# Optimization experiments

Hardware: AMD Instinct MI355X
Metric: run time of the kernel (lower is better)

Reference implementation:

```python
import jax, jax.numpy as jnp
import numpy as np

RHO, MU, DT = 1.0, 0.1, 4.0
AX_X, AX_Y = -1, -2  # x = last axis, y = second-to-last


def first_derivative(f, ax, scheme):
    # unit grid spacing; boundary wrap is irrelevant since [1:-1,1:-1] is sliced off
    if scheme == 'left':
        return f - jnp.roll(f, 1, ax)
    if scheme == 'right':
        return jnp.roll(f, -1, ax) - f
    return 0.5 * (jnp.roll(f, -1, ax) - jnp.roll(f, 1, ax))  # central


def vel_map(f, ax, side):
    # staggered-grid interpolation of velocity to neighboring face
    if side == 'left':
        return 0.5 * (f + jnp.roll(f, 1, ax))
    return 0.5 * (f + jnp.roll(f, -1, ax))


def laplacian(f):
    return (jnp.roll(f, 1, AX_X) + jnp.roll(f, -1, AX_X)
            + jnp.roll(f, 1, AX_Y) + jnp.roll(f, -1, AX_Y) - 4.0 * f)


def setup_inputs() -> dict:
    key = jax.random.key(0)
    k1, k2, k3, k4 = jax.random.split(key, 4)
    B, H, W = 8, 1024, 1024
    return {
        'v_old': jax.random.normal(k1, (B, 2, H, W), dtype=jnp.float32),
        'v_new': jax.random.normal(k2, (B, 2, H, W), dtype=jnp.float32),
        'p_new': jax.random.normal(k3, (B, 1, H, W), dtype=jnp.float32),
        'flow_mask_mac': jax.random.randint(k4, (B, 1, H, W), 0, 2).astype(jnp.int32),
    }


def reference(v_old, v_new, p_new, flow_mask_mac):
    mask = flow_mask_mac.astype(v_old.dtype)
    v = 0.5 * (v_new + v_old)  # integration == 'imex'

    u_old, w_old = v_old[:, 0:1], v_old[:, 1:2]
    u_new, w_new = v_new[:, 0:1], v_new[:, 1:2]
    u, w = v[:, 0:1], v[:, 1:2]

    # x-momentum residual (channel 1)
    res_x = mask * (RHO * ((w_new - w_old) / DT
                           + w * first_derivative(w, AX_X, 'central')
                           + 0.5 * (vel_map(u, AX_X, 'left') * first_derivative(w, AX_Y, 'left')
                                    + vel_map(u, AX_X, 'right') * first_derivative(w, AX_Y, 'right')))
                    + first_derivative(p_new, AX_X, 'left')
                    - MU * laplacian(w))

    # y-momentum residual (channel 0)
    res_y = mask * (RHO * ((u_new - u_old) / DT
                           + u * first_derivative(u, AX_Y, 'central')
                           + 0.5 * (vel_map(w, AX_Y, 'left') * first_derivative(u, AX_X, 'left')
                                    + vel_map(w, AX_Y, 'right') * first_derivative(u, AX_X, 'right')))
                    + first_derivative(p_new, AX_Y, 'left')
                    - MU * laplacian(u))

    loss_x = jnp.mean(jnp.square(res_x)[:, :, 1:-1, 1:-1], axis=(1, 2, 3))
    loss_y = jnp.mean(jnp.square(res_y)[:, :, 1:-1, 1:-1], axis=(1, 2, 3))
    return loss_x + loss_y  # shape [B]
```

## Files before the change

### kernel.cpp

```cpp
#include <hip/hip_runtime.h>


#define NS_H 1024
#define NS_W 1024
#define RPB 2
#define PAIRS ((NS_H - 2) / RPB)
#define PARTS_PER_B PAIRS

__device__ __forceinline__ float4 ld4(const float* p) { return *(const float4*)p; }
__device__ __forceinline__ int4  ld4i(const int* p)   { return *(const int4*)p; }
__device__ __forceinline__ float4 avg4(float4 a, float4 b) {
    return make_float4(0.5f*(a.x+b.x), 0.5f*(a.y+b.y), 0.5f*(a.z+b.z), 0.5f*(a.w+b.w));
}
__device__ __forceinline__ float4 sub4(float4 a, float4 b) {
    return make_float4(a.x-b.x, a.y-b.y, a.z-b.z, a.w-b.w);
}

__global__ __launch_bounds__(256, 3) void ns_loss_partial(
    const float* __restrict__ v_old,
    const float* __restrict__ v_new,
    const float* __restrict__ p,
    const int*   __restrict__ mask,
    float* __restrict__ ws)
{
    const int blkp = blockIdx.x;
    const int lg   = (blkp & 7) * PAIRS + (blkp >> 3);
    const int b    = lg / PAIRS;
    const int pr   = lg % PAIRS;
    const int y    = 1 + pr * RPB;

    const size_t hw = (size_t)NS_H * NS_W;
    const float* uo = v_old + (size_t)b * 2 * hw;
    const float* wo = uo + hw;
    const float* un = v_new + (size_t)b * 2 * hw;
    const float* wn = un + hw;
    const float* pb = p    + (size_t)b * hw;
    const int*   mb = mask + (size_t)b * hw;

    const int tid  = (int)threadIdx.x;
    const int lane = tid & 63;
    const int wid  = tid >> 6;
    const int x0   = tid * 4;
    const bool has_r = (x0 + 4 < NS_W);

    const int rm  = (y - 1) * NS_W;
    const int rc  = y * NS_W;
    const int rp  = rc + NS_W;
    const int rpp = rp + NS_W;

    float4 un_m = ld4(un + rm  + x0), uo_m = ld4(uo + rm  + x0);
    float4 un_c = ld4(un + rc  + x0), uo_c = ld4(uo + rc  + x0);
    float4 un_p = ld4(un + rp  + x0), uo_p = ld4(uo + rp  + x0);
    float4 un_q = ld4(un + rpp + x0), uo_q = ld4(uo + rpp + x0);
    float4 wn_m = ld4(wn + rm  + x0), wo_m = ld4(wo + rm  + x0);
    float4 wn_c = ld4(wn + rc  + x0), wo_c = ld4(wo + rc  + x0);
    float4 wn_p = ld4(wn + rp  + x0), wo_p = ld4(wo + rp  + x0);
    float4 wn_q = ld4(wn + rpp + x0), wo_q = ld4(wo + rpp + x0);
    float4 p_m4 = ld4(pb + rm + x0);
    float4 p_c4 = ld4(pb + rc + x0);
    float4 p_p4 = ld4(pb + rp + x0);
    int4   m_c4 = ld4i(mb + rc + x0);
    int4   m_p4 = ld4i(mb + rp + x0);
    __builtin_amdgcn_sched_barrier(0);

    float4 u_m = avg4(un_m, uo_m), u_c = avg4(un_c, uo_c);
    float4 u_p = avg4(un_p, uo_p), u_q = avg4(un_q, uo_q);
    float4 w_m = avg4(wn_m, wo_m), w_c = avg4(wn_c, wo_c);
    float4 w_p = avg4(wn_p, wo_p), w_q = avg4(wn_q, wo_q);
    float4 du_c = sub4(un_c, uo_c), du_p = sub4(un_p, uo_p);
    float4 dw_c = sub4(wn_c, wo_c), dw_p = sub4(wn_p, wo_p);

    __shared__ float edge[4][10];
    if (lane == 63) {
        edge[wid][0] = u_c.w;  edge[wid][1] = w_c.w;  edge[wid][2] = p_c4.w;
        edge[wid][3] = u_p.w;  edge[wid][4] = w_p.w;  edge[wid][5] = p_p4.w;
    }
    if (lane == 0) {
        edge[wid][6] = u_c.x;  edge[wid][7] = w_c.x;
        edge[wid][8] = u_p.x;  edge[wid][9] = w_p.x;
    }
    __syncthreads();

    float ul_c = __shfl_up(u_c.w, 1),  wl_c = __shfl_up(w_c.w, 1);
    float ul_p = __shfl_up(u_p.w, 1),  wl_p = __shfl_up(w_p.w, 1);
    float pl_c = __shfl_up(p_c4.w, 1), pl_p = __shfl_up(p_p4.w, 1);
    if (lane == 0 && wid > 0) {
        ul_c = edge[wid-1][0]; wl_c = edge[wid-1][1]; pl_c = edge[wid-1][2];
        ul_p = edge[wid-1][3]; wl_p = edge[wid-1][4]; pl_p = edge[wid-1][5];
    }
    float ur_c = __shfl_down(u_c.x, 1), wr_c = __shfl_down(w_c.x, 1);
    float ur_p = __shfl_down(u_p.x, 1), wr_p = __shfl_down(w_p.x, 1);
    if (lane == 63 && wid < 3) {
        ur_c = edge[wid+1][6]; wr_c = edge[wid+1][7];
        ur_p = edge[wid+1][8]; wr_p = edge[wid+1][9];
    }
    if (!has_r) { ur_c = 0.f; wr_c = 0.f; ur_p = 0.f; wr_p = 0.f; }

    float acc = 0.f;

    {
        const float uc[6]  = {ul_c, u_c.x, u_c.y, u_c.z, u_c.w, ur_c};
        const float wcv[6] = {wl_c, w_c.x, w_c.y, w_c.z, w_c.w, wr_c};
        const float uym[4] = {u_m.x, u_m.y, u_m.z, u_m.w};
        const float uyp[4] = {u_p.x, u_p.y, u_p.z, u_p.w};
        const float wym[4] = {w_m.x, w_m.y, w_m.z, w_m.w};
        const float wyp[4] = {w_p.x, w_p.y, w_p.z, w_p.w};
        const float du[4]  = {du_c.x, du_c.y, du_c.z, du_c.w};
        const float dw[4]  = {dw_c.x, dw_c.y, dw_c.z, dw_c.w};
        const float pcv[5] = {pl_c, p_c4.x, p_c4.y, p_c4.z, p_c4.w};
        const float pym[4] = {p_m4.x, p_m4.y, p_m4.z, p_m4.w};
        const int   mm[4]  = {m_c4.x, m_c4.y, m_c4.z, m_c4.w};

        #pragma unroll
        for (int j = 0; j < 4; ++j) {
            const int x = x0 + j;
            const float m = (x >= 1 && x <= NS_W - 2) ? (float)mm[j] : 0.f;
            const float u_cc = uc[j+1],  u_xm = uc[j],  u_xp = uc[j+2];
            const float w_cc = wcv[j+1], w_xm = wcv[j], w_xp = wcv[j+2];

            float res_x =
                dw[j] * 0.25f
              + w_cc * 0.5f * (w_xp - w_xm)
              + 0.5f * ( 0.5f * (u_cc + u_xm) * (w_cc   - wym[j])
                       + 0.5f * (u_cc + u_xp) * (wyp[j] - w_cc  ) )
              + (pcv[j+1] - pcv[j])
              - 0.1f * (w_xm + w_xp + wym[j] + wyp[j] - 4.f * w_cc);

            float res_y =
                du[j] * 0.25f
              + u_cc * 0.5f * (uyp[j] - uym[j])
              + 0.5f * ( 0.5f * (w_cc + wym[j]) * (u_cc - u_xm)
                       + 0.5f * (w_cc + wyp[j]) * (u_xp - u_cc) )
              + (pcv[j+1] - pym[j])
              - 0.1f * (u_xm + u_xp + uym[j] + uyp[j] - 4.f * u_cc);

            acc += m * (res_x * res_x + res_y * res_y);
        }
    }

    {
        const float uc[6]  = {ul_p, u_p.x, u_p.y, u_p.z, u_p.w, ur_p};
        const float wcv[6] = {wl_p, w_p.x, w_p.y, w_p.z, w_p.w, wr_p};
        const float uym[4] = {u_c.x, u_c.y, u_c.z, u_c.w};
        const float uyp[4] = {u_q.x, u_q.y, u_q.z, u_q.w};
        const float wym[4] = {w_c.x, w_c.y, w_c.z, w_c.w};
        const float wyp[4] = {w_q.x, w_q.y, w_q.z, w_q.w};
        const float du[4]  = {du_p.x, du_p.y, du_p.z, du_p.w};
        const float dw[4]  = {dw_p.x, dw_p.y, dw_p.z, dw_p.w};
        const float pcv[5] = {pl_p, p_p4.x, p_p4.y, p_p4.z, p_p4.w};
        const float pym[4] = {p_c4.x, p_c4.y, p_c4.z, p_c4.w};
        const int   mm[4]  = {m_p4.x, m_p4.y, m_p4.z, m_p4.w};

        #pragma unroll
        for (int j = 0; j < 4; ++j) {
            const int x = x0 + j;
            const float m = (x >= 1 && x <= NS_W - 2) ? (float)mm[j] : 0.f;
            const float u_cc = uc[j+1],  u_xm = uc[j],  u_xp = uc[j+2];
            const float w_cc = wcv[j+1], w_xm = wcv[j], w_xp = wcv[j+2];

            float res_x =
                dw[j] * 0.25f
              + w_cc * 0.5f * (w_xp - w_xm)
              + 0.5f * ( 0.5f * (u_cc + u_xm) * (w_cc   - wym[j])
                       + 0.5f * (u_cc + u_xp) * (wyp[j] - w_cc  ) )
              + (pcv[j+1] - pcv[j])
              - 0.1f * (w_xm + w_xp + wym[j] + wyp[j] - 4.f * w_cc);

            float res_y =
                du[j] * 0.25f
              + u_cc * 0.5f * (uyp[j] - uym[j])
              + 0.5f * ( 0.5f * (w_cc + wym[j]) * (u_cc - u_xm)
                       + 0.5f * (w_cc + wyp[j]) * (u_xp - u_cc) )
              + (pcv[j+1] - pym[j])
              - 0.1f * (u_xm + u_xp + uym[j] + uyp[j] - 4.f * u_cc);

            acc += m * (res_x * res_x + res_y * res_y);
        }
    }

    #pragma unroll
    for (int off = 32; off > 0; off >>= 1)
        acc += __shfl_down(acc, off);

    __shared__ float smem[4];
    if (lane == 0) smem[wid] = acc;
    __syncthreads();

    if (tid == 0)
        ws[lg] = smem[0] + smem[1] + smem[2] + smem[3];
}

__global__ __launch_bounds__(256) void ns_loss_reduce(
    const float* __restrict__ ws, float* __restrict__ out)
{
    const int b = blockIdx.x;
    float acc = 0.f;
    for (int i = threadIdx.x; i < PARTS_PER_B; i += 256)
        acc += ws[b * PARTS_PER_B + i];

    #pragma unroll
    for (int off = 32; off > 0; off >>= 1)
        acc += __shfl_down(acc, off);

    __shared__ float smem[4];
    const int lane = threadIdx.x & 63;
    const int wid  = threadIdx.x >> 6;
    if (lane == 0) smem[wid] = acc;
    __syncthreads();

    if (threadIdx.x == 0) {
        const float inv = 1.0f / ((float)(NS_H - 2) * (float)(NS_W - 2));
        out[b] = (smem[0] + smem[1] + smem[2] + smem[3]) * inv;
    }
}

extern "C" void kernel_launch(void* const* d_in, const int* in_sizes, int n_in,
                              void* d_out, int out_size, void* d_ws, size_t ws_size,
                              hipStream_t stream) {
    const float* v_old = (const float*)d_in[0];
    const float* v_new = (const float*)d_in[1];
    const float* p_new = (const float*)d_in[2];
    const int*   msk   = (const int*)d_in[3];
    float* out = (float*)d_out;
    float* ws  = (float*)d_ws;

    const int B = out_size;

    ns_loss_partial<<<dim3(B * PAIRS), dim3(256), 0, stream>>>(v_old, v_new, p_new, msk, ws);
    ns_loss_reduce<<<dim3(B), dim3(256), 0, stream>>>(ws, out);
}
```

Before: 200.4 us.

## Process four rows per block with a second staged load batch

Each block now handles four interior rows instead of two, so the halo rows of velocity loaded from global memory are shared across more output rows. The loads for the third and fourth rows are issued before the first pair is computed, so they overlap with that arithmetic. Rows past the interior are clamped and masked with validity factors. The cost is higher register pressure under the launch bound of three blocks, fewer blocks in the grid, and a second shared-memory edge exchange with its own barrier.

```diff
diff --git a/kernel.cpp b/kernel.cpp
--- a/kernel.cpp
+++ b/kernel.cpp
@@ -3,9 +3,9 @@
 
 #define NS_H 1024
 #define NS_W 1024
-#define RPB 2
-#define PAIRS ((NS_H - 2) / RPB)
-#define PARTS_PER_B PAIRS
+#define RPB 4
+#define NBY 256
+#define PARTS_PER_B NBY
 
 __device__ __forceinline__ float4 ld4(const float* p) { return *(const float4*)p; }
 __device__ __forceinline__ int4  ld4i(const int* p)   { return *(const int4*)p; }
@@ -24,10 +24,10 @@
     float* __restrict__ ws)
 {
     const int blkp = blockIdx.x;
-    const int lg   = (blkp & 7) * PAIRS + (blkp >> 3);
-    const int b    = lg / PAIRS;
-    const int pr   = lg % PAIRS;
-    const int y    = 1 + pr * RPB;
+    const int lg   = (blkp & 7) * NBY + (blkp >> 3);
+    const int b    = lg / NBY;
+    const int cy   = lg % NBY;
+    const int y0   = 1 + cy * RPB;
 
     const size_t hw = (size_t)NS_H * NS_W;
     const float* uo = v_old + (size_t)b * 2 * hw;
@@ -41,21 +41,29 @@
     const int lane = tid & 63;
     const int wid  = tid >> 6;
     const int x0   = tid * 4;
-    const bool has_r = (x0 + 4 < NS_W);
-
-    const int rm  = (y - 1) * NS_W;
-    const int rc  = y * NS_W;
+    const bool has_r = (tid != 255);
+
+    const int rm  = (y0 - 1) * NS_W;
+    const int rc  = rm + NS_W;
     const int rp  = rc + NS_W;
-    const int rpp = rp + NS_W;
-
-    float4 un_m = ld4(un + rm  + x0), uo_m = ld4(uo + rm  + x0);
-    float4 un_c = ld4(un + rc  + x0), uo_c = ld4(uo + rc  + x0);
-    float4 un_p = ld4(un + rp  + x0), uo_p = ld4(uo + rp  + x0);
-    float4 un_q = ld4(un + rpp + x0), uo_q = ld4(uo + rpp + x0);
-    float4 wn_m = ld4(wn + rm  + x0), wo_m = ld4(wo + rm  + x0);
-    float4 wn_c = ld4(wn + rc  + x0), wo_c = ld4(wo + rc  + x0);
-    float4 wn_p = ld4(wn + rp  + x0), wo_p = ld4(wo + rp  + x0);
-    float4 wn_q = ld4(wn + rpp + x0), wo_q = ld4(wo + rpp + x0);
+    const int rq  = rp + NS_W;
+    int Rr = y0 + 3; if (Rr > 1023) Rr = 1023;
+    int Rs = y0 + 4; if (Rs > 1023) Rs = 1023;
+    const int rr = Rr * NS_W;
+    const int rs = Rs * NS_W;
+    const float rv_q = (y0 + 2 <= NS_H - 2) ? 1.f : 0.f;
+    const float rv_r = (y0 + 3 <= NS_H - 2) ? 1.f : 0.f;
+
+    __shared__ float edge[2][4][10];
+
+    float4 un_m = ld4(un + rm + x0), uo_m = ld4(uo + rm + x0);
+    float4 un_c = ld4(un + rc + x0), uo_c = ld4(uo + rc + x0);
+    float4 un_p = ld4(un + rp + x0), uo_p = ld4(uo + rp + x0);
+    float4 un_q = ld4(un + rq + x0), uo_q = ld4(uo + rq + x0);
+    float4 wn_m = ld4(wn + rm + x0), wo_m = ld4(wo + rm + x0);
+    float4 wn_c = ld4(wn + rc + x0), wo_c = ld4(wo + rc + x0);
+    float4 wn_p = ld4(wn + rp + x0), wo_p = ld4(wo + rp + x0);
+    float4 wn_q = ld4(wn + rq + x0), wo_q = ld4(wo + rq + x0);
     float4 p_m4 = ld4(pb + rm + x0);
     float4 p_c4 = ld4(pb + rc + x0);
     float4 p_p4 = ld4(pb + rp + x0);
@@ -69,15 +77,15 @@
     float4 w_p = avg4(wn_p, wo_p), w_q = avg4(wn_q, wo_q);
     float4 du_c = sub4(un_c, uo_c), du_p = sub4(un_p, uo_p);
     float4 dw_c = sub4(wn_c, wo_c), dw_p = sub4(wn_p, wo_p);
-
-    __shared__ float edge[4][10];
+    float4 du_q = sub4(un_q, uo_q), dw_q = sub4(wn_q, wo_q);
+
     if (lane == 63) {
-        edge[wid][0] = u_c.w;  edge[wid][1] = w_c.w;  edge[wid][2] = p_c4.w;
-        edge[wid][3] = u_p.w;  edge[wid][4] = w_p.w;  edge[wid][5] = p_p4.w;
+        edge[0][wid][0] = u_c.w;  edge[0][wid][1] = w_c.w;  edge[0][wid][2] = p_c4.w;
+        edge[0][wid][3] = u_p.w;  edge[0][wid][4] = w_p.w;  edge[0][wid][5] = p_p4.w;
     }
     if (lane == 0) {
-        edge[wid][6] = u_c.x;  edge[wid][7] = w_c.x;
-        edge[wid][8] = u_p.x;  edge[wid][9] = w_p.x;
+        edge[0][wid][6] = u_c.x;  edge[0][wid][7] = w_c.x;
+        edge[0][wid][8] = u_p.x;  edge[0][wid][9] = w_p.x;
     }
     __syncthreads();
 
@@ -85,16 +93,26 @@
     float ul_p = __shfl_up(u_p.w, 1),  wl_p = __shfl_up(w_p.w, 1);
     float pl_c = __shfl_up(p_c4.w, 1), pl_p = __shfl_up(p_p4.w, 1);
     if (lane == 0 && wid > 0) {
-        ul_c = edge[wid-1][0]; wl_c = edge[wid-1][1]; pl_c = edge[wid-1][2];
-        ul_p = edge[wid-1][3]; wl_p = edge[wid-1][4]; pl_p = edge[wid-1][5];
+        ul_c = edge[0][wid-1][0]; wl_c = edge[0][wid-1][1]; pl_c = edge[0][wid-1][2];
+        ul_p = edge[0][wid-1][3]; wl_p = edge[0][wid-1][4]; pl_p = edge[0][wid-1][5];
     }
     float ur_c = __shfl_down(u_c.x, 1), wr_c = __shfl_down(w_c.x, 1);
     float ur_p = __shfl_down(u_p.x, 1), wr_p = __shfl_down(w_p.x, 1);
     if (lane == 63 && wid < 3) {
-        ur_c = edge[wid+1][6]; wr_c = edge[wid+1][7];
-        ur_p = edge[wid+1][8]; wr_p = edge[wid+1][9];
+        ur_c = edge[0][wid+1][6]; wr_c = edge[0][wid+1][7];
+        ur_p = edge[0][wid+1][8]; wr_p = edge[0][wid+1][9];
     }
     if (!has_r) { ur_c = 0.f; wr_c = 0.f; ur_p = 0.f; wr_p = 0.f; }
+
+    float4 un_r = ld4(un + rr + x0), uo_r = ld4(uo + rr + x0);
+    float4 wn_r = ld4(wn + rr + x0), wo_r = ld4(wo + rr + x0);
+    float4 un_s = ld4(un + rs + x0), uo_s = ld4(uo + rs + x0);
+    float4 wn_s = ld4(wn + rs + x0), wo_s = ld4(wo + rs + x0);
+    float4 p_q4 = ld4(pb + rq + x0);
+    float4 p_r4 = ld4(pb + rr + x0);
+    int4   m_q4 = ld4i(mb + rq + x0);
+    int4   m_r4 = ld4i(mb + rr + x0);
+    __builtin_amdgcn_sched_barrier(0);
 
     float acc = 0.f;
 
@@ -178,6 +196,115 @@
         }
     }
 
+    float4 u_r = avg4(un_r, uo_r), w_r = avg4(wn_r, wo_r);
+    float4 du_r = sub4(un_r, uo_r), dw_r = sub4(wn_r, wo_r);
+    float4 u_s = avg4(un_s, uo_s), w_s = avg4(wn_s, wo_s);
+
+    if (lane == 63) {
+        edge[1][wid][0] = u_q.w;  edge[1][wid][1] = w_q.w;  edge[1][wid][2] = p_q4.w;
+        edge[1][wid][3] = u_r.w;  edge[1][wid][4] = w_r.w;  edge[1][wid][5] = p_r4.w;
+    }
+    if (lane == 0) {
+        edge[1][wid][6] = u_q.x;  edge[1][wid][7] = w_q.x;
+        edge[1][wid][8] = u_r.x;  edge[1][wid][9] = w_r.x;
+    }
+    __syncthreads();
+
+    float ul_q = __shfl_up(u_q.w, 1),  wl_q = __shfl_up(w_q.w, 1);
+    float ul_r = __shfl_up(u_r.w, 1),  wl_r = __shfl_up(w_r.w, 1);
+    float pl_q = __shfl_up(p_q4.w, 1), pl_r = __shfl_up(p_r4.w, 1);
+    if (lane == 0 && wid > 0) {
+        ul_q = edge[1][wid-1][0]; wl_q = edge[1][wid-1][1]; pl_q = edge[1][wid-1][2];
+        ul_r = edge[1][wid-1][3]; wl_r = edge[1][wid-1][4]; pl_r = edge[1][wid-1][5];
+    }
+    float ur_q = __shfl_down(u_q.x, 1), wr_q = __shfl_down(w_q.x, 1);
+    float ur_r = __shfl_down(u_r.x, 1), wr_r = __shfl_down(w_r.x, 1);
+    if (lane == 63 && wid < 3) {
+        ur_q = edge[1][wid+1][6]; wr_q = edge[1][wid+1][7];
+        ur_r = edge[1][wid+1][8]; wr_r = edge[1][wid+1][9];
+    }
+    if (!has_r) { ur_q = 0.f; wr_q = 0.f; ur_r = 0.f; wr_r = 0.f; }
+
+    {
+        const float uc[6]  = {ul_q, u_q.x, u_q.y, u_q.z, u_q.w, ur_q};
+        const float wcv[6] = {wl_q, w_q.x, w_q.y, w_q.z, w_q.w, wr_q};
+        const float uym[4] = {u_p.x, u_p.y, u_p.z, u_p.w};
+        const float uyp[4] = {u_r.x, u_r.y, u_r.z, u_r.w};
+        const float wym[4] = {w_p.x, w_p.y, w_p.z, w_p.w};
+        const float wyp[4] = {w_r.x, w_r.y, w_r.z, w_r.w};
+        const float du[4]  = {du_q.x, du_q.y, du_q.z, du_q.w};
+        const float dw[4]  = {dw_q.x, dw_q.y, dw_q.z, dw_q.w};
+        const float pcv[5] = {pl_q, p_q4.x, p_q4.y, p_q4.z, p_q4.w};
+        const float pym[4] = {p_p4.x, p_p4.y, p_p4.z, p_p4.w};
+        const int   mm[4]  = {m_q4.x, m_q4.y, m_q4.z, m_q4.w};
+
+        #pragma unroll
+        for (int j = 0; j < 4; ++j) {
+            const int x = x0 + j;
+            const float m = ((x >= 1 && x <= NS_W - 2) ? (float)mm[j] : 0.f) * rv_q;
+            const float u_cc = uc[j+1],  u_xm = uc[j],  u_xp = uc[j+2];
+            const float w_cc = wcv[j+1], w_xm = wcv[j], w_xp = wcv[j+2];
+
+            float res_x =
+                dw[j] * 0.25f
+              + w_cc * 0.5f * (w_xp - w_xm)
+              + 0.5f * ( 0.5f * (u_cc + u_xm) * (w_cc   - wym[j])
+                       + 0.5f * (u_cc + u_xp) * (wyp[j] - w_cc  ) )
+              + (pcv[j+1] - pcv[j])
+              - 0.1f * (w_xm + w_xp + wym[j] + wyp[j] - 4.f * w_cc);
+
+            float res_y =
+                du[j] * 0.25f
+              + u_cc * 0.5f * (uyp[j] - uym[j])
+              + 0.5f * ( 0.5f * (w_cc + wym[j]) * (u_cc - u_xm)
+                       + 0.5f * (w_cc + wyp[j]) * (u_xp - u_cc) )
+              + (pcv[j+1] - pym[j])
+              - 0.1f * (u_xm + u_xp + uym[j] + uyp[j] - 4.f * u_cc);
+
+            acc += m * (res_x * res_x + res_y * res_y);
+        }
+    }
+
+    {
+        const float uc[6]  = {ul_r, u_r.x, u_r.y, u_r.z, u_r.w, ur_r};
+        const float wcv[6] = {wl_r, w_r.x, w_r.y, w_r.z, w_r.w, wr_r};
+        const float uym[4] = {u_q.x, u_q.y, u_q.z, u_q.w};
+        const float uyp[4] = {u_s.x, u_s.y, u_s.z, u_s.w};
+        const float wym[4] = {w_q.x, w_q.y, w_q.z, w_q.w};
+        const float wyp[4] = {w_s.x, w_s.y, w_s.z, w_s.w};
+        const float du[4]  = {du_r.x, du_r.y, du_r.z, du_r.w};
+        const float dw[4]  = {dw_r.x, dw_r.y, dw_r.z, dw_r.w};
+        const float pcv[5] = {pl_r, p_r4.x, p_r4.y, p_r4.z, p_r4.w};
+        const float pym[4] = {p_q4.x, p_q4.y, p_q4.z, p_q4.w};
+        const int   mm[4]  = {m_r4.x, m_r4.y, m_r4.z, m_r4.w};
+
+        #pragma unroll
+        for (int j = 0; j < 4; ++j) {
+            const int x = x0 + j;
+            const float m = ((x >= 1 && x <= NS_W - 2) ? (float)mm[j] : 0.f) * rv_r;
+            const float u_cc = uc[j+1],  u_xm = uc[j],  u_xp = uc[j+2];
+            const float w_cc = wcv[j+1], w_xm = wcv[j], w_xp = wcv[j+2];
+
+            float res_x =
+                dw[j] * 0.25f
+              + w_cc * 0.5f * (w_xp - w_xm)
+              + 0.5f * ( 0.5f * (u_cc + u_xm) * (w_cc   - wym[j])
+                       + 0.5f * (u_cc + u_xp) * (wyp[j] - w_cc  ) )
+              + (pcv[j+1] - pcv[j])
+              - 0.1f * (w_xm + w_xp + wym[j] + wyp[j] - 4.f * w_cc);
+
+            float res_y =
+                du[j] * 0.25f
+              + u_cc * 0.5f * (uyp[j] - uym[j])
+              + 0.5f * ( 0.5f * (w_cc + wym[j]) * (u_cc - u_xm)
+                       + 0.5f * (w_cc + wyp[j]) * (u_xp - u_cc) )
+              + (pcv[j+1] - pym[j])
+              - 0.1f * (u_xm + u_xp + uym[j] + uyp[j] - 4.f * u_cc);
+
+            acc += m * (res_x * res_x + res_y * res_y);
+        }
+    }
+
     #pragma unroll
     for (int off = 32; off > 0; off >>= 1)
         acc += __shfl_down(acc, off);
@@ -226,6 +353,6 @@
 
     const int B = out_size;
 
-    ns_loss_partial<<<dim3(B * PAIRS), dim3(256), 0, stream>>>(v_old, v_new, p_new, msk, ws);
+    ns_loss_partial<<<dim3(B * NBY), dim3(256), 0, stream>>>(v_old, v_new, p_new, msk, ws);
     ns_loss_reduce<<<dim3(B), dim3(256), 0, stream>>>(ws, out);
 }
```

New measurement: 209.5 us. 1.05x slower.
